# Kernel optimization log

Measured on AMD Instinct MI355X. Metric: run time of the kernel, lower is better.

Reference implementation:

```python
import jax, jax.numpy as jnp
import numpy as np

B, L, D, H = 4, 96, 256, 8
HD = D // H
FF = 4 * D
EPS = 1e-5


def _layernorm(x, g, b):
    m = jnp.mean(x, axis=-1, keepdims=True)
    v = jnp.mean((x - m) ** 2, axis=-1, keepdims=True)
    return (x - m) * jax.lax.rsqrt(v + EPS) * g + b


def setup_inputs() -> dict:
    key = jax.random.key(0)
    ks = jax.random.split(key, 12)

    def w(k, shape, fan_in):
        return jax.random.normal(k, shape, jnp.float32) / np.sqrt(fan_in)

    return {
        "table": jax.random.normal(ks[0], (B, L, L, D), jnp.float32),
        "dep_matrix": jax.random.uniform(ks[1], (B, L, L), jnp.float32),
        "Wq": w(ks[2], (D, D), D), "bq": jnp.zeros((D,), jnp.float32),
        "Wk": w(ks[3], (D, D), D), "bk": jnp.zeros((D,), jnp.float32),
        "Wv": w(ks[4], (D, D), D), "bv": jnp.zeros((D,), jnp.float32),
        "Wo": w(ks[5], (D, D), D), "bo": jnp.zeros((D,), jnp.float32),
        "Wdep": w(ks[6], (1, H), 1), "bdep": jnp.zeros((H,), jnp.float32),
        "ln1_g": jnp.ones((D,), jnp.float32), "ln1_b": jnp.zeros((D,), jnp.float32),
        "W1": w(ks[7], (D, FF), D), "b1": jnp.zeros((FF,), jnp.float32),
        "W2": w(ks[8], (FF, D), FF), "b2": jnp.zeros((D,), jnp.float32),
        "ln2_g": jnp.ones((D,), jnp.float32), "ln2_b": jnp.zeros((D,), jnp.float32),
    }


def reference(table, dep_matrix, Wq, bq, Wk, bk, Wv, bv, Wo, bo, Wdep, bdep,
              ln1_g, ln1_b, W1, b1, W2, b2, ln2_g, ln2_b):
    Bx, Lx, _, Dx = table.shape
    Hh = bdep.shape[0]
    hd = Dx // Hh

    def proj(W, b):  # [B,L,L,D] -> [B,H,L,L,hd]
        return (table @ W + b).reshape(Bx, Lx, Lx, Hh, hd).transpose(0, 3, 1, 2, 4)

    q, k, v = proj(Wq, bq), proj(Wk, bk), proj(Wv, bv)

    # attention over last L axis, batched over (B, H, first-L):  [B,H,L,L,L]
    scores = jnp.einsum('bhxqd,bhxkd->bhxqk', q, k) / np.sqrt(hd)

    # learned dependency bias: Linear(1 -> H) on dep_matrix, broadcast over q axis
    dep = dep_matrix[..., None] * Wdep[0] + bdep          # [B,L,L,H]
    dep = dep.transpose(0, 3, 1, 2)[:, :, :, None, :]      # [B,H,L,1,L]

    probs = jax.nn.softmax(scores + dep, axis=-1)          # dropout = identity (eval)

    ctx = jnp.einsum('bhxqk,bhxkd->bhxqd', probs, v)       # [B,H,L,L,hd]
    ctx = ctx.transpose(0, 2, 3, 1, 4).reshape(Bx, Lx, Lx, Dx)

    out = _layernorm(ctx @ Wo + bo + table, ln1_g, ln1_b)
    ff = jax.nn.relu(out @ W1 + b1) @ W2 + b2
    return _layernorm(ff + out, ln2_g, ln2_b)
```

## Files before the change

kernel.cpp:

```cpp
#include <hip/hip_runtime.h>
#include <hip/hip_bf16.h>
#include <math.h>

#define M_ROWS 36864

typedef __bf16 bf16x8 __attribute__((ext_vector_type(8)));
typedef __bf16 bf16x4 __attribute__((ext_vector_type(4)));
typedef float f32x4 __attribute__((ext_vector_type(4)));

__device__ __forceinline__ void gload16(const void* g, void* l) {
  __builtin_amdgcn_global_load_lds((const __attribute__((address_space(1))) void*)g,
                                   (__attribute__((address_space(3))) void*)l, 16, 0, 0);
}

__global__ __launch_bounds__(256) void pack_w_kernel(
    const float* __restrict__ Wq, const float* __restrict__ Wk, const float* __restrict__ Wv,
    const float* __restrict__ Wo, const float* __restrict__ W1, const float* __restrict__ W2,
    const float* __restrict__ bq, const float* __restrict__ bk, const float* __restrict__ bv,
    __bf16* __restrict__ Wqkv_t, __bf16* __restrict__ Wo_t,
    __bf16* __restrict__ W1_t, __bf16* __restrict__ W2_t, float* __restrict__ bqkv) {
  int idx = blockIdx.x * 256 + threadIdx.x;
  const int S1 = 768 * 256, S2 = 256 * 256, S3 = 1024 * 256;
  if (idx < S1) {
    int n = idx / 256, k = idx % 256;
    int sel = n >> 8, nn = n & 255;
    const float* W = (sel == 0) ? Wq : (sel == 1) ? Wk : Wv;
    Wqkv_t[idx] = (__bf16)W[k * 256 + nn];
  } else if (idx < S1 + S2) {
    int j = idx - S1; int n = j / 256, k = j % 256;
    Wo_t[j] = (__bf16)Wo[k * 256 + n];
  } else if (idx < S1 + S2 + S3) {
    int j = idx - S1 - S2; int n = j / 256, k = j % 256;
    W1_t[j] = (__bf16)W1[k * 1024 + n];
  } else {
    int j = idx - S1 - S2 - S3; int n = j / 1024, k = j % 1024;
    W2_t[j] = (__bf16)W2[k * 256 + n];
  }
  if (idx < 768) {
    int sel = idx >> 8, jj = idx & 255;
    const float* bsrc = (sel == 0) ? bq : (sel == 1) ? bk : bv;
    bqkv[idx] = bsrc[jj];
  }
}

template <int EPI, bool AF32>
__global__ __launch_bounds__(256, 4) void gemm_k64_kernel(
    const void* __restrict__ Av, const __bf16* __restrict__ Bt,
    const float* __restrict__ bias, __hip_bfloat16* __restrict__ Y, int N, int K) {
  __shared__ __bf16 As[64 * 64];
  __shared__ __bf16 Bs[128 * 64];
  const int tid = threadIdx.x;
  const int lane = tid & 63, wv = tid >> 6;
  const int wm = wv >> 1, wn = wv & 1;
  const int gx = gridDim.x;
  const int nwg = gx * gridDim.y;
  int lin = blockIdx.y * gx + blockIdx.x;
  lin = (lin & 7) * (nwg >> 3) + (lin >> 3);
  const int n0 = (lin % gx) * 128;
  const int m0 = (lin / gx) * 64;
  const int fr = lane & 15, g = lane >> 4;
  const int lrow8 = lane >> 3;
  const int gs = (lane & 7) ^ lrow8;
  const int gseg = gs * 8;

  f32x4 acc[2][4] = {};
  const int nph = K >> 6;

  for (int p = 0; p < nph; ++p) {
    const int kb = p * 64;
    __syncthreads();
    if (AF32) {
      const float* Af = (const float*)Av;
      const float* s0 = &Af[(size_t)(m0 + wv * 16 + lrow8) * K + kb + gseg];
      const float* s1 = &Af[(size_t)(m0 + wv * 16 + 8 + lrow8) * K + kb + gseg];
      float4 a0 = *(const float4*)s0, a1 = *(const float4*)(s0 + 4);
      float4 b0 = *(const float4*)s1, b1 = *(const float4*)(s1 + 4);
      bf16x8 o0 = {(__bf16)a0.x, (__bf16)a0.y, (__bf16)a0.z, (__bf16)a0.w,
                   (__bf16)a1.x, (__bf16)a1.y, (__bf16)a1.z, (__bf16)a1.w};
      bf16x8 o1 = {(__bf16)b0.x, (__bf16)b0.y, (__bf16)b0.z, (__bf16)b0.w,
                   (__bf16)b1.x, (__bf16)b1.y, (__bf16)b1.z, (__bf16)b1.w};
      *(bf16x8*)&As[wv * 1024 + lane * 8] = o0;
      *(bf16x8*)&As[wv * 1024 + 512 + lane * 8] = o1;
    } else {
      const __bf16* Ab = (const __bf16*)Av;
      gload16(Ab + (size_t)(m0 + wv * 16 + lrow8) * K + kb + gseg,     &As[wv * 1024]);
      gload16(Ab + (size_t)(m0 + wv * 16 + 8 + lrow8) * K + kb + gseg, &As[wv * 1024 + 512]);
    }
#pragma unroll
    for (int j = 0; j < 4; ++j)
      gload16(Bt + (size_t)(n0 + wv * 32 + j * 8 + lrow8) * K + kb + gseg,
              &Bs[wv * 2048 + j * 512]);
    __syncthreads();
#pragma unroll
    for (int s = 0; s < 2; ++s) {
      bf16x8 av[2], bv[4];
      const int cs = ((s * 4 + g) ^ (fr & 7)) * 8;
#pragma unroll
      for (int mi = 0; mi < 2; ++mi)
        av[mi] = *reinterpret_cast<const bf16x8*>(&As[(wm * 32 + mi * 16 + fr) * 64 + cs]);
#pragma unroll
      for (int ni = 0; ni < 4; ++ni)
        bv[ni] = *reinterpret_cast<const bf16x8*>(&Bs[(wn * 64 + ni * 16 + fr) * 64 + cs]);
#pragma unroll
      for (int mi = 0; mi < 2; ++mi)
#pragma unroll
        for (int ni = 0; ni < 4; ++ni)
          acc[mi][ni] = __builtin_amdgcn_mfma_f32_16x16x32_bf16(av[mi], bv[ni], acc[mi][ni], 0, 0, 0);
    }
  }

  const int crow = m0 + wm * 32 + g * 4;
  const int ccol = n0 + wn * 64 + fr;
#pragma unroll
  for (int mi = 0; mi < 2; ++mi) {
#pragma unroll
    for (int ni = 0; ni < 4; ++ni) {
      const int col = ccol + ni * 16;
      const float bb = bias[col];
#pragma unroll
      for (int r = 0; r < 4; ++r) {
        const int row = crow + mi * 16 + r;
        float v = acc[mi][ni][r] + bb;
        if (EPI == 1) v = fmaxf(v, 0.f);
        Y[(size_t)row * N + col] = __float2bfloat16(v);
      }
    }
  }
}

template <bool RESID_F32, bool OUT_F32>
__global__ __launch_bounds__(256, 4) void gemm_ln32_kernel(
    const __bf16* __restrict__ A, const __bf16* __restrict__ Bt,
    const float* __restrict__ bias, const void* __restrict__ residv,
    const float* __restrict__ gamma, const float* __restrict__ beta,
    void* __restrict__ Y, int K) {
  __shared__ __bf16 As[32 * 64];
  __shared__ __bf16 Bs[256 * 64];
  __shared__ float red[2][4][32];
  const int tid = threadIdx.x;
  const int lane = tid & 63, wv = tid >> 6;
  const int nwg = gridDim.x;
  int lin = blockIdx.x;
  lin = (lin & 7) * (nwg >> 3) + (lin >> 3);
  const int m0 = lin * 32;
  const int fr = lane & 15, g = lane >> 4;
  const int lrow8 = lane >> 3;
  const int gseg = ((lane & 7) ^ lrow8) * 8;

  f32x4 acc[2][4] = {};
  const int nph = K >> 6;

  for (int p = 0; p < nph; ++p) {
    const int kb = p * 64;
    __syncthreads();
    gload16(A + (size_t)(m0 + wv * 8 + lrow8) * K + kb + gseg, &As[wv * 512]);
#pragma unroll
    for (int j = 0; j < 8; ++j)
      gload16(Bt + (size_t)(wv * 64 + j * 8 + lrow8) * K + kb + gseg,
              &Bs[wv * 4096 + j * 512]);
    __syncthreads();
#pragma unroll
    for (int s = 0; s < 2; ++s) {
      bf16x8 av[2], bv[4];
      const int cs = ((s * 4 + g) ^ (fr & 7)) * 8;
#pragma unroll
      for (int mi = 0; mi < 2; ++mi)
        av[mi] = *reinterpret_cast<const bf16x8*>(&As[(mi * 16 + fr) * 64 + cs]);
#pragma unroll
      for (int ni = 0; ni < 4; ++ni)
        bv[ni] = *reinterpret_cast<const bf16x8*>(&Bs[(wv * 64 + ni * 16 + fr) * 64 + cs]);
#pragma unroll
      for (int mi = 0; mi < 2; ++mi)
#pragma unroll
        for (int ni = 0; ni < 4; ++ni)
          acc[mi][ni] = __builtin_amdgcn_mfma_f32_16x16x32_bf16(av[mi], bv[ni], acc[mi][ni], 0, 0, 0);
    }
  }

  const int colb = wv * 64 + fr;
  float bb[4], gg[4], be[4];
#pragma unroll
  for (int ni = 0; ni < 4; ++ni) {
    bb[ni] = bias[colb + ni * 16];
    gg[ni] = gamma[colb + ni * 16];
    be[ni] = beta[colb + ni * 16];
  }
#pragma unroll
  for (int mi = 0; mi < 2; ++mi) {
#pragma unroll
    for (int r = 0; r < 4; ++r) {
      const int lr = mi * 16 + g * 4 + r;
      const size_t grow = (size_t)(m0 + lr) * 256;
      float s = 0.f, q = 0.f;
#pragma unroll
      for (int ni = 0; ni < 4; ++ni) {
        const int col = colb + ni * 16;
        const float rr = RESID_F32 ? ((const float*)residv)[grow + col]
                                   : (float)((const __bf16*)residv)[grow + col];
        float v = acc[mi][ni][r] + bb[ni] + rr;
        acc[mi][ni][r] = v;
        s += v; q += v * v;
      }
#pragma unroll
      for (int o = 8; o > 0; o >>= 1) { s += __shfl_xor(s, o); q += __shfl_xor(q, o); }
      if (fr == 0) { red[0][wv][lr] = s; red[1][wv][lr] = q; }
    }
  }
  __syncthreads();
#pragma unroll
  for (int mi = 0; mi < 2; ++mi) {
#pragma unroll
    for (int r = 0; r < 4; ++r) {
      const int lr = mi * 16 + g * 4 + r;
      const size_t grow = (size_t)(m0 + lr) * 256;
      const float s = red[0][0][lr] + red[0][1][lr] + red[0][2][lr] + red[0][3][lr];
      const float q = red[1][0][lr] + red[1][1][lr] + red[1][2][lr] + red[1][3][lr];
      const float mean = s * (1.0f / 256.0f);
      const float var = q * (1.0f / 256.0f) - mean * mean;
      const float inv = rsqrtf(var + 1e-5f);
#pragma unroll
      for (int ni = 0; ni < 4; ++ni) {
        const float y = (acc[mi][ni][r] - mean) * inv * gg[ni] + be[ni];
        if (OUT_F32) ((float*)Y)[grow + colb + ni * 16] = y;
        else ((__hip_bfloat16*)Y)[grow + colb + ni * 16] = __float2bfloat16(y);
      }
    }
  }
}

__global__ __launch_bounds__(384) void attn_mfma_kernel(
    const __bf16* __restrict__ qkv, const float* __restrict__ depm,
    const float* __restrict__ Wdep, const float* __restrict__ bdep,
    __hip_bfloat16* __restrict__ ctx) {
  __shared__ __bf16 Qs[96][40];
  __shared__ __bf16 Ks[96][40];
  __shared__ __bf16 Vt[32][104];
  __shared__ __bf16 Ps[6][16][104];
  int lin = blockIdx.x;
  lin = (lin & 7) * 384 + (lin >> 3);
  const int h = lin & 7;
  const int sx = lin >> 3;
  const int x = sx % 96;
  const int b = sx / 96;
  const int tid = threadIdx.x;
  const size_t slab = (size_t)(b * 96 + x) * 96;
  const size_t base = slab * 768 + h * 32;
#pragma unroll
  for (int t = 0; t < 3; ++t) {
    const int idx = tid + t * 384;
    const int r = idx / 12, rem = idx % 12, mat = rem >> 2, seg = rem & 3;
    const int d0 = seg * 8;
    bf16x8 v8 = *(const bf16x8*)&qkv[base + (size_t)r * 768 + mat * 256 + d0];
    if (mat == 0)      *(bf16x8*)&Qs[r][d0] = v8;
    else if (mat == 1) *(bf16x8*)&Ks[r][d0] = v8;
    else {
#pragma unroll
      for (int e = 0; e < 8; ++e) Vt[d0 + e][r] = v8[e];
    }
  }
  __syncthreads();
  const int wave = tid >> 6, lane = tid & 63;
  const int fr = lane & 15, g = lane >> 4;
  const int q0 = wave * 16;
  const float wd = Wdep[h], bd = bdep[h];
  float depb[6];
#pragma unroll
  for (int f = 0; f < 6; ++f) depb[f] = depm[slab + fr + 16 * f] * wd + bd;
  const bf16x8 av = *(const bf16x8*)&Qs[q0 + fr][g * 8];
  f32x4 sacc[6];
#pragma unroll
  for (int f = 0; f < 6; ++f) {
    const bf16x8 bv = *(const bf16x8*)&Ks[f * 16 + fr][g * 8];
    sacc[f] = __builtin_amdgcn_mfma_f32_16x16x32_bf16(av, bv, (f32x4){0.f, 0.f, 0.f, 0.f}, 0, 0, 0);
  }
  const float scale = 0.17677669529663687f;
  float ev[6][4];
  float inv[4];
#pragma unroll
  for (int r = 0; r < 4; ++r) {
    float m = -1e30f;
#pragma unroll
    for (int f = 0; f < 6; ++f) {
      ev[f][r] = sacc[f][r] * scale + depb[f];
      m = fmaxf(m, ev[f][r]);
    }
#pragma unroll
    for (int o = 8; o > 0; o >>= 1) m = fmaxf(m, __shfl_xor(m, o));
    float sum = 0.f;
#pragma unroll
    for (int f = 0; f < 6; ++f) { ev[f][r] = __expf(ev[f][r] - m); sum += ev[f][r]; }
#pragma unroll
    for (int o = 8; o > 0; o >>= 1) sum += __shfl_xor(sum, o);
    inv[r] = 1.0f / sum;
  }
#pragma unroll
  for (int f = 0; f < 6; ++f)
#pragma unroll
    for (int r = 0; r < 4; ++r)
      Ps[wave][g * 4 + r][fr + 16 * f] = (__bf16)ev[f][r];
  asm volatile("s_waitcnt lgkmcnt(0)" ::: "memory");
  f32x4 o0 = {0.f, 0.f, 0.f, 0.f}, o1 = {0.f, 0.f, 0.f, 0.f};
#pragma unroll
  for (int s = 0; s < 3; ++s) {
    const bf16x8 pa  = *(const bf16x8*)&Ps[wave][fr][s * 32 + g * 8];
    const bf16x8 vb0 = *(const bf16x8*)&Vt[fr][s * 32 + g * 8];
    const bf16x8 vb1 = *(const bf16x8*)&Vt[16 + fr][s * 32 + g * 8];
    o0 = __builtin_amdgcn_mfma_f32_16x16x32_bf16(pa, vb0, o0, 0, 0, 0);
    o1 = __builtin_amdgcn_mfma_f32_16x16x32_bf16(pa, vb1, o1, 0, 0, 0);
  }
  const size_t orow = (slab + q0 + g * 4) * 256 + h * 32;
#pragma unroll
  for (int r = 0; r < 4; ++r) {
    ctx[orow + (size_t)r * 256 + fr]      = __float2bfloat16(o0[r] * inv[r]);
    ctx[orow + (size_t)r * 256 + 16 + fr] = __float2bfloat16(o1[r] * inv[r]);
  }
}

extern "C" void kernel_launch(void* const* d_in, const int* in_sizes, int n_in,
                              void* d_out, int out_size, void* d_ws, size_t ws_size,
                              hipStream_t stream) {
  (void)in_sizes; (void)n_in; (void)out_size; (void)ws_size;
  const float* table = (const float*)d_in[0];
  const float* depm  = (const float*)d_in[1];
  const float* Wq = (const float*)d_in[2];   const float* bq = (const float*)d_in[3];
  const float* Wk = (const float*)d_in[4];   const float* bk = (const float*)d_in[5];
  const float* Wv = (const float*)d_in[6];   const float* bv = (const float*)d_in[7];
  const float* Wo = (const float*)d_in[8];   const float* bo = (const float*)d_in[9];
  const float* Wdep = (const float*)d_in[10]; const float* bdep = (const float*)d_in[11];
  const float* g1 = (const float*)d_in[12];  const float* be1 = (const float*)d_in[13];
  const float* W1 = (const float*)d_in[14];  const float* b1 = (const float*)d_in[15];
  const float* W2 = (const float*)d_in[16];  const float* b2 = (const float*)d_in[17];
  const float* g2 = (const float*)d_in[18];  const float* be2 = (const float*)d_in[19];

  char* ws = (char*)d_ws;
  size_t off = 0;
  __bf16* qkvb  = (__bf16*)(ws + off); off += (size_t)M_ROWS * 768 * 2;
  __bf16* ctxb  = (__bf16*)(ws + off); off += (size_t)M_ROWS * 256 * 2;
  __bf16* outbb = (__bf16*)(ws + off); off += (size_t)M_ROWS * 256 * 2;
  __bf16* hidb  = (__bf16*)(ws + off); off += (size_t)M_ROWS * 1024 * 2;
  __bf16* Wqkv_t = (__bf16*)(ws + off); off += 768 * 256 * 2;
  __bf16* Wo_t   = (__bf16*)(ws + off); off += 256 * 256 * 2;
  __bf16* W1_t   = (__bf16*)(ws + off); off += 1024 * 256 * 2;
  __bf16* W2_t   = (__bf16*)(ws + off); off += 256 * 1024 * 2;
  float*  bqkv   = (float*)(ws + off);

  pack_w_kernel<<<3072, 256, 0, stream>>>(Wq, Wk, Wv, Wo, W1, W2, bq, bk, bv,
                                          Wqkv_t, Wo_t, W1_t, W2_t, bqkv);
  gemm_k64_kernel<0, true><<<dim3(6, 576), 256, 0, stream>>>(
      table, Wqkv_t, bqkv, (__hip_bfloat16*)qkvb, 768, 256);
  attn_mfma_kernel<<<3072, 384, 0, stream>>>(qkvb, depm, Wdep, bdep, (__hip_bfloat16*)ctxb);
  gemm_ln32_kernel<true, false><<<1152, 256, 0, stream>>>(
      ctxb, Wo_t, bo, table, g1, be1, outbb, 256);
  gemm_k64_kernel<1, false><<<dim3(8, 576), 256, 0, stream>>>(
      outbb, W1_t, b1, (__hip_bfloat16*)hidb, 1024, 256);
  gemm_ln32_kernel<false, true><<<1152, 256, 0, stream>>>(
      hidb, W2_t, b2, outbb, g2, be2, (float*)d_out, 1024);
}
```

Baseline: 175.2 us.

## Double-buffer FFN1 GEMM with K=32 tiles and widen LN GEMM to 64 rows

Adds a gemm_small kernel for the W1 GEMM. It uses K-step 32 tiles with double-buffered LDS staging, so the next tile's global loads overlap the current MFMA work. The LayerNorm-fused GEMMs now process 64 rows per block instead of 32, with the grid halved, which doubles the reuse of the loaded 256-column weight tile. The cost is more accumulator registers, with occupancy lowered to 3 waves, and fewer workgroups.

```diff
diff --git a/kernel.cpp b/kernel.cpp
--- a/kernel.cpp
+++ b/kernel.cpp
@@ -60,8 +60,7 @@
   const int m0 = (lin / gx) * 64;
   const int fr = lane & 15, g = lane >> 4;
   const int lrow8 = lane >> 3;
-  const int gs = (lane & 7) ^ lrow8;
-  const int gseg = gs * 8;
+  const int gseg = ((lane & 7) ^ lrow8) * 8;
 
   f32x4 acc[2][4] = {};
   const int nph = K >> 6;
@@ -128,32 +127,109 @@
   }
 }
 
+template <int EPI>
+__global__ __launch_bounds__(256, 4) void gemm_small_kernel(
+    const __bf16* __restrict__ A, const __bf16* __restrict__ Bt,
+    const float* __restrict__ bias, const __bf16* __restrict__ resid,
+    __hip_bfloat16* __restrict__ Y, int N, int K) {
+  __shared__ __bf16 As[2][64 * 32];
+  __shared__ __bf16 Bs[2][128 * 32];
+  const int tid = threadIdx.x;
+  const int lane = tid & 63, wv = tid >> 6;
+  const int wm = wv >> 1, wn = wv & 1;
+  const int gx = gridDim.x;
+  const int nwg = gx * gridDim.y;
+  int lin = blockIdx.y * gx + blockIdx.x;
+  lin = (lin & 7) * (nwg >> 3) + (lin >> 3);
+  const int n0 = (lin % gx) * 128;
+  const int m0 = (lin / gx) * 64;
+  const int fr = lane & 15, g = lane >> 4;
+  const int rrel = lane >> 2;
+  const int gsegA = ((lane & 3) ^ ((lane >> 3) & 3)) * 8;
+
+  f32x4 acc[2][4] = {};
+  const int nph = K >> 5;
+
+#define STAGE_S(buf, kb)                                                        \
+  {                                                                             \
+    gload16(A + (size_t)(m0 + wv * 16 + rrel) * K + (kb) + gsegA,               \
+            &As[buf][wv * 512]);                                                \
+    gload16(Bt + (size_t)(n0 + wv * 16 + rrel) * K + (kb) + gsegA,              \
+            &Bs[buf][wv * 512]);                                                \
+    gload16(Bt + (size_t)(n0 + 64 + wv * 16 + rrel) * K + (kb) + gsegA,         \
+            &Bs[buf][2048 + wv * 512]);                                         \
+  }
+
+  STAGE_S(0, 0)
+  __syncthreads();
+  int cur = 0;
+  for (int p = 0; p < nph; ++p) {
+    if (p + 1 < nph) STAGE_S(cur ^ 1, (p + 1) * 32)
+    const int cs = (g ^ ((fr >> 1) & 3)) * 8;
+    bf16x8 av[2], bv[4];
+#pragma unroll
+    for (int mi = 0; mi < 2; ++mi)
+      av[mi] = *reinterpret_cast<const bf16x8*>(&As[cur][(wm * 32 + mi * 16 + fr) * 32 + cs]);
+#pragma unroll
+    for (int ni = 0; ni < 4; ++ni)
+      bv[ni] = *reinterpret_cast<const bf16x8*>(&Bs[cur][(wn * 64 + ni * 16 + fr) * 32 + cs]);
+#pragma unroll
+    for (int mi = 0; mi < 2; ++mi)
+#pragma unroll
+      for (int ni = 0; ni < 4; ++ni)
+        acc[mi][ni] = __builtin_amdgcn_mfma_f32_16x16x32_bf16(av[mi], bv[ni], acc[mi][ni], 0, 0, 0);
+    __syncthreads();
+    cur ^= 1;
+  }
+#undef STAGE_S
+
+  const int crow = m0 + wm * 32 + g * 4;
+  const int ccol = n0 + wn * 64 + fr;
+#pragma unroll
+  for (int mi = 0; mi < 2; ++mi) {
+#pragma unroll
+    for (int ni = 0; ni < 4; ++ni) {
+      const int col = ccol + ni * 16;
+      const float bb = bias[col];
+#pragma unroll
+      for (int r = 0; r < 4; ++r) {
+        const int row = crow + mi * 16 + r;
+        float v = acc[mi][ni][r] + bb;
+        if (EPI == 1) v = fmaxf(v, 0.f);
+        if (EPI == 2) v += (float)resid[(size_t)row * N + col];
+        Y[(size_t)row * N + col] = __float2bfloat16(v);
+      }
+    }
+  }
+}
+
 template <bool RESID_F32, bool OUT_F32>
-__global__ __launch_bounds__(256, 4) void gemm_ln32_kernel(
+__global__ __launch_bounds__(256, 3) void gemm_ln256_kernel(
     const __bf16* __restrict__ A, const __bf16* __restrict__ Bt,
     const float* __restrict__ bias, const void* __restrict__ residv,
     const float* __restrict__ gamma, const float* __restrict__ beta,
     void* __restrict__ Y, int K) {
-  __shared__ __bf16 As[32 * 64];
+  __shared__ __bf16 As[64 * 64];
   __shared__ __bf16 Bs[256 * 64];
-  __shared__ float red[2][4][32];
+  __shared__ float red[2][4][64];
   const int tid = threadIdx.x;
   const int lane = tid & 63, wv = tid >> 6;
   const int nwg = gridDim.x;
   int lin = blockIdx.x;
   lin = (lin & 7) * (nwg >> 3) + (lin >> 3);
-  const int m0 = lin * 32;
+  const int m0 = lin * 64;
   const int fr = lane & 15, g = lane >> 4;
   const int lrow8 = lane >> 3;
   const int gseg = ((lane & 7) ^ lrow8) * 8;
 
-  f32x4 acc[2][4] = {};
+  f32x4 acc[4][4] = {};
   const int nph = K >> 6;
 
   for (int p = 0; p < nph; ++p) {
     const int kb = p * 64;
     __syncthreads();
-    gload16(A + (size_t)(m0 + wv * 8 + lrow8) * K + kb + gseg, &As[wv * 512]);
+    gload16(A + (size_t)(m0 + wv * 16 + lrow8) * K + kb + gseg,     &As[wv * 1024]);
+    gload16(A + (size_t)(m0 + wv * 16 + 8 + lrow8) * K + kb + gseg, &As[wv * 1024 + 512]);
 #pragma unroll
     for (int j = 0; j < 8; ++j)
       gload16(Bt + (size_t)(wv * 64 + j * 8 + lrow8) * K + kb + gseg,
@@ -161,16 +237,16 @@
     __syncthreads();
 #pragma unroll
     for (int s = 0; s < 2; ++s) {
-      bf16x8 av[2], bv[4];
+      bf16x8 av[4], bv[4];
       const int cs = ((s * 4 + g) ^ (fr & 7)) * 8;
 #pragma unroll
-      for (int mi = 0; mi < 2; ++mi)
+      for (int mi = 0; mi < 4; ++mi)
         av[mi] = *reinterpret_cast<const bf16x8*>(&As[(mi * 16 + fr) * 64 + cs]);
 #pragma unroll
       for (int ni = 0; ni < 4; ++ni)
         bv[ni] = *reinterpret_cast<const bf16x8*>(&Bs[(wv * 64 + ni * 16 + fr) * 64 + cs]);
 #pragma unroll
-      for (int mi = 0; mi < 2; ++mi)
+      for (int mi = 0; mi < 4; ++mi)
 #pragma unroll
         for (int ni = 0; ni < 4; ++ni)
           acc[mi][ni] = __builtin_amdgcn_mfma_f32_16x16x32_bf16(av[mi], bv[ni], acc[mi][ni], 0, 0, 0);
@@ -186,7 +262,7 @@
     be[ni] = beta[colb + ni * 16];
   }
 #pragma unroll
-  for (int mi = 0; mi < 2; ++mi) {
+  for (int mi = 0; mi < 4; ++mi) {
 #pragma unroll
     for (int r = 0; r < 4; ++r) {
       const int lr = mi * 16 + g * 4 + r;
@@ -208,7 +284,7 @@
   }
   __syncthreads();
 #pragma unroll
-  for (int mi = 0; mi < 2; ++mi) {
+  for (int mi = 0; mi < 4; ++mi) {
 #pragma unroll
     for (int r = 0; r < 4; ++r) {
       const int lr = mi * 16 + g * 4 + r;
@@ -349,10 +425,10 @@
   gemm_k64_kernel<0, true><<<dim3(6, 576), 256, 0, stream>>>(
       table, Wqkv_t, bqkv, (__hip_bfloat16*)qkvb, 768, 256);
   attn_mfma_kernel<<<3072, 384, 0, stream>>>(qkvb, depm, Wdep, bdep, (__hip_bfloat16*)ctxb);
-  gemm_ln32_kernel<true, false><<<1152, 256, 0, stream>>>(
+  gemm_ln256_kernel<true, false><<<576, 256, 0, stream>>>(
       ctxb, Wo_t, bo, table, g1, be1, outbb, 256);
-  gemm_k64_kernel<1, false><<<dim3(8, 576), 256, 0, stream>>>(
-      outbb, W1_t, b1, (__hip_bfloat16*)hidb, 1024, 256);
-  gemm_ln32_kernel<false, true><<<1152, 256, 0, stream>>>(
+  gemm_small_kernel<1><<<dim3(8, 576), 256, 0, stream>>>(
+      outbb, W1_t, b1, nullptr, (__hip_bfloat16*)hidb, 1024, 256);
+  gemm_ln256_kernel<false, true><<<576, 256, 0, stream>>>(
       hidb, W2_t, b2, outbb, g2, be2, (float*)d_out, 1024);
 }
```

Result: no change. 173.4 us (-1.0%).
